# Performance work log

Measured on AMD Instinct MI355X. Metric: run time of the kernel, lower is better.

Reference implementation:

```python
import jax, jax.numpy as jnp
import numpy as np

N, C, INTER = 8192, 256, 128


def setup_inputs() -> dict:
    key = jax.random.key(0)
    ks = jax.random.split(key, 9)
    s_in = 1.0 / np.sqrt(C)
    s_mid = 1.0 / np.sqrt(INTER)
    return {
        "x": jax.random.normal(ks[0], (N, C), dtype=jnp.float32),
        # weights stored [in, out] so projection is x @ w + b
        "g_w": jax.random.uniform(ks[1], (C, INTER), jnp.float32, -s_in, s_in),
        "g_b": jax.random.uniform(ks[2], (INTER,), jnp.float32, -s_in, s_in),
        "theta_w": jax.random.uniform(ks[3], (C, INTER), jnp.float32, -s_in, s_in),
        "theta_b": jax.random.uniform(ks[4], (INTER,), jnp.float32, -s_in, s_in),
        "phi_w": jax.random.uniform(ks[5], (C, INTER), jnp.float32, -s_in, s_in),
        "phi_b": jax.random.uniform(ks[6], (INTER,), jnp.float32, -s_in, s_in),
        "W_w": jax.random.uniform(ks[7], (INTER, C), jnp.float32, -s_mid, s_mid),
        "W_b": jax.random.uniform(ks[8], (C,), jnp.float32, -s_mid, s_mid),
    }


def reference(x, g_w, g_b, theta_w, theta_b, phi_w, phi_b, W_w, W_b):
    # embedded_gaussian variant; dropout treated as eval-mode identity
    g_x = x @ g_w + g_b            # [N, inter]
    theta_x = x @ theta_w + theta_b  # [N, inter]
    phi_x = x @ phi_w + phi_b        # [N, inter]
    f = theta_x @ phi_x.T            # [N, N] score matrix
    f_div_C = jax.nn.softmax(f, axis=-1)
    y = f_div_C @ g_x                # [N, inter]
    W_y = y @ W_w + W_b              # [N, C]
    return W_y + x
```

## Files before the change

kernel.cpp:

```cpp
#include <hip/hip_runtime.h>


typedef __bf16 bf16x8 __attribute__((ext_vector_type(8)));
typedef __bf16 bf16x4 __attribute__((ext_vector_type(4)));
typedef float f32x16 __attribute__((ext_vector_type(16)));

#define DEV __device__ __forceinline__

constexpr int NROW = 8192;
constexpr int CDIM = 256;
constexpr int DI   = 128;
constexpr int KVS  = 8;

DEV int crow(int r, int h) { return (r & 3) + 8 * (r >> 2) + 4 * h; }

DEV f32x16 mfma(bf16x8 a, bf16x8 b, f32x16 c) {
    return __builtin_amdgcn_mfma_f32_32x32x16_bf16(a, b, c, 0, 0, 0);
}

__global__ __launch_bounds__(256, 2) void proj_nt(
    const float* __restrict__ x, const float* __restrict__ w,
    const float* __restrict__ bias, __bf16* __restrict__ out)
{
    __shared__ __align__(16) __bf16 Wl[CDIM * DI];
    const int tid = threadIdx.x;
    const int wv = tid >> 6, lane = tid & 63, l31 = lane & 31, h = lane >> 5;

#pragma unroll
    for (int j = 0; j < 32; ++j) {
        int cid = j * 256 + tid;
        float4 v = ((const float4*)w)[cid];
        bf16x4 t;
        t[0] = (__bf16)v.x; t[1] = (__bf16)v.y; t[2] = (__bf16)v.z; t[3] = (__bf16)v.w;
        *(bf16x4*)(&Wl[cid * 4]) = t;
    }
    __syncthreads();

    const int row0 = blockIdx.x * 128 + wv * 32;
    f32x16 acc[4] = {};

#pragma unroll
    for (int kk = 0; kk < 16; ++kk) {
        const float4* xp = (const float4*)(x + (size_t)(row0 + l31) * CDIM + kk * 16 + h * 8);
        float4 a0 = xp[0], a1 = xp[1];
        bf16x8 af;
        af[0] = (__bf16)a0.x; af[1] = (__bf16)a0.y; af[2] = (__bf16)a0.z; af[3] = (__bf16)a0.w;
        af[4] = (__bf16)a1.x; af[5] = (__bf16)a1.y; af[6] = (__bf16)a1.z; af[7] = (__bf16)a1.w;
#pragma unroll
        for (int jn = 0; jn < 4; ++jn) {
            bf16x8 bf;
#pragma unroll
            for (int u = 0; u < 8; ++u)
                bf[u] = Wl[(kk * 16 + h * 8 + u) * DI + jn * 32 + l31];
            acc[jn] = mfma(af, bf, acc[jn]);
        }
    }

#pragma unroll
    for (int jn = 0; jn < 4; ++jn) {
        int col = jn * 32 + l31;
        float bv = bias[col];
#pragma unroll
        for (int r = 0; r < 16; ++r) {
            int row = row0 + crow(r, h);
            out[(size_t)row * DI + col] = (__bf16)(acc[jn][r] + bv);
        }
    }
}

__global__ __launch_bounds__(256, 2) void proj_gT(
    const float* __restrict__ x, const float* __restrict__ w,
    const float* __restrict__ bias, __bf16* __restrict__ outT)
{
    __shared__ __align__(16) __bf16 Wl[CDIM * DI];
    const int tid = threadIdx.x;
    const int wv = tid >> 6, lane = tid & 63, l31 = lane & 31, h = lane >> 5;

#pragma unroll
    for (int j = 0; j < 32; ++j) {
        int cid = j * 256 + tid;
        float4 v = ((const float4*)w)[cid];
        bf16x4 t;
        t[0] = (__bf16)v.x; t[1] = (__bf16)v.y; t[2] = (__bf16)v.z; t[3] = (__bf16)v.w;
        *(bf16x4*)(&Wl[cid * 4]) = t;
    }
    __syncthreads();

    const int n0 = blockIdx.x * 128;
    f32x16 acc[4] = {};

#pragma unroll
    for (int kk = 0; kk < 16; ++kk) {
        bf16x8 af;
#pragma unroll
        for (int u = 0; u < 8; ++u)
            af[u] = Wl[(kk * 16 + h * 8 + u) * DI + wv * 32 + l31];
#pragma unroll
        for (int jn = 0; jn < 4; ++jn) {
            const float4* xp = (const float4*)(x + (size_t)(n0 + jn * 32 + l31) * CDIM + kk * 16 + h * 8);
            float4 b0 = xp[0], b1 = xp[1];
            bf16x8 bf;
            bf[0] = (__bf16)b0.x; bf[1] = (__bf16)b0.y; bf[2] = (__bf16)b0.z; bf[3] = (__bf16)b0.w;
            bf[4] = (__bf16)b1.x; bf[5] = (__bf16)b1.y; bf[6] = (__bf16)b1.z; bf[7] = (__bf16)b1.w;
            acc[jn] = mfma(af, bf, acc[jn]);
        }
    }

#pragma unroll
    for (int jn = 0; jn < 4; ++jn) {
        int xr = n0 + jn * 32 + l31;
#pragma unroll
        for (int r = 0; r < 16; ++r) {
            int i = wv * 32 + crow(r, h);
            outT[(size_t)i * NROW + xr] = (__bf16)(acc[jn][r] + bias[i]);
        }
    }
}

__global__ __launch_bounds__(256, 2) void flash(
    const __bf16* __restrict__ q, const __bf16* __restrict__ k,
    const __bf16* __restrict__ vT, float* __restrict__ yaccT,
    float* __restrict__ mlm, float* __restrict__ mll)
{
    __shared__ __align__(16) __bf16 Kt[64 * 128];
    __shared__ __align__(16) __bf16 Vt[64 * 128];
    __shared__ __align__(16) __bf16 Pl[4][32 * 64];

    const int tid = threadIdx.x;
    const int wv = tid >> 6, lane = tid & 63, l31 = lane & 31, h = lane >> 5;
    const int qt = blockIdx.x, sp = blockIdx.y;
    const int q0 = qt * 128 + wv * 32;

    bf16x8 qf[8];
#pragma unroll
    for (int kk = 0; kk < 8; ++kk)
        qf[kk] = *(const bf16x8*)(q + (size_t)(q0 + l31) * DI + kk * 16 + h * 8);

    f32x16 yacc[4] = {};
    float m = -1e30f, l = 0.f;

    for (int it = 0; it < 16; ++it) {
        const int kvb = sp * (NROW / KVS) + it * 64;

#pragma unroll
        for (int j = 0; j < 4; ++j) {
            int cid = j * 256 + tid;
            int r = cid >> 4, dc = (cid & 15) * 8;
            bf16x8 val = *(const bf16x8*)(k + (size_t)(kvb + r) * DI + dc);
            *(bf16x8*)(&Kt[(r * 128 + dc) ^ ((r & 15) << 3)]) = val;
        }
#pragma unroll
        for (int j = 0; j < 4; ++j) {
            int cid = j * 256 + tid;
            int d = cid >> 3, kvc = (cid & 7) * 8;
            bf16x8 val = *(const bf16x8*)(vT + (size_t)d * NROW + kvb + kvc);
            int rw = d >> 1, co = (d & 1) * 64 + kvc;
            *(bf16x8*)(&Vt[(rw * 128 + co) ^ ((rw & 15) << 3)]) = val;
        }
        __syncthreads();

        f32x16 sacc[2] = {};
#pragma unroll
        for (int kk = 0; kk < 8; ++kk) {
#pragma unroll
            for (int jm = 0; jm < 2; ++jm) {
                int kv = jm * 32 + l31;
                bf16x8 kf = *(const bf16x8*)(&Kt[(kv * 128 + kk * 16 + h * 8) ^ ((kv & 15) << 3)]);
                sacc[jm] = mfma(kf, qf[kk], sacc[jm]);
            }
        }

        float tm = -1e30f;
#pragma unroll
        for (int jm = 0; jm < 2; ++jm)
#pragma unroll
            for (int r = 0; r < 16; ++r) tm = fmaxf(tm, sacc[jm][r]);
        tm = fmaxf(tm, __shfl_xor(tm, 32));
        float mn = fmaxf(m, tm);
        float scale = __expf(m - mn);
        float ts = 0.f;
#pragma unroll
        for (int jm = 0; jm < 2; ++jm)
#pragma unroll
            for (int r = 0; r < 16; ++r) {
                float p = __expf(sacc[jm][r] - mn);
                sacc[jm][r] = p;
                ts += p;
            }
        ts += __shfl_xor(ts, 32);
        m = mn;
        l = l * scale + ts;
#pragma unroll
        for (int jd = 0; jd < 4; ++jd) yacc[jd] *= scale;

#pragma unroll
        for (int jm = 0; jm < 2; ++jm)
#pragma unroll
            for (int r = 0; r < 16; ++r) {
                int kv = jm * 32 + crow(r, h);
                Pl[wv][(l31 * 64 + kv) ^ ((l31 & 7) << 3)] = (__bf16)sacc[jm][r];
            }
        __syncthreads();

        bf16x8 pf[4];
#pragma unroll
        for (int ks = 0; ks < 4; ++ks)
            pf[ks] = *(const bf16x8*)(&Pl[wv][(l31 * 64 + ks * 16 + h * 8) ^ ((l31 & 7) << 3)]);
#pragma unroll
        for (int jd = 0; jd < 4; ++jd) {
            int d = jd * 32 + l31, rw = d >> 1;
#pragma unroll
            for (int ks = 0; ks < 4; ++ks) {
                int co = (d & 1) * 64 + ks * 16 + h * 8;
                bf16x8 vf = *(const bf16x8*)(&Vt[(rw * 128 + co) ^ ((rw & 15) << 3)]);
                yacc[jd] = mfma(vf, pf[ks], yacc[jd]);
            }
        }
        __syncthreads();
    }

#pragma unroll
    for (int jd = 0; jd < 4; ++jd)
#pragma unroll
        for (int r = 0; r < 16; ++r) {
            int d = jd * 32 + crow(r, h);
            yaccT[(size_t)sp * DI * NROW + (size_t)d * NROW + qt * 128 + wv * 32 + l31] = yacc[jd][r];
        }
    if (h == 0) {
        mlm[sp * NROW + q0 + l31] = m;
        mll[sp * NROW + q0 + l31] = l;
    }
}

__global__ void merge_y(const float* __restrict__ yaccT,
                        const float* __restrict__ mlm, const float* __restrict__ mll,
                        __bf16* __restrict__ y)
{
    int idx = blockIdx.x * 256 + threadIdx.x;
    int d = idx >> 13, qq = idx & 8191;
    float ms[KVS];
    float m = -1e30f;
#pragma unroll
    for (int s = 0; s < KVS; ++s) {
        ms[s] = mlm[s * NROW + qq];
        m = fmaxf(m, ms[s]);
    }
    float L = 0.f, acc = 0.f;
#pragma unroll
    for (int s = 0; s < KVS; ++s) {
        float e = __expf(ms[s] - m);
        L += mll[s * NROW + qq] * e;
        acc += e * yaccT[(size_t)s * DI * NROW + (size_t)d * NROW + qq];
    }
    y[(size_t)qq * DI + d] = (__bf16)(acc / L);
}

__global__ __launch_bounds__(256, 2) void final_proj(
    const __bf16* __restrict__ y, const float* __restrict__ w,
    const float* __restrict__ bias, const float* __restrict__ x,
    float* __restrict__ out)
{
    __shared__ __align__(16) __bf16 Wl[DI * CDIM];
    const int tid = threadIdx.x;
    const int wv = tid >> 6, lane = tid & 63, l31 = lane & 31, h = lane >> 5;

#pragma unroll
    for (int j = 0; j < 32; ++j) {
        int cid = j * 256 + tid;
        float4 v = ((const float4*)w)[cid];
        bf16x4 t;
        t[0] = (__bf16)v.x; t[1] = (__bf16)v.y; t[2] = (__bf16)v.z; t[3] = (__bf16)v.w;
        *(bf16x4*)(&Wl[cid * 4]) = t;
    }
    __syncthreads();

    const int row0 = blockIdx.x * 128 + wv * 32;
    bf16x8 af[8];
#pragma unroll
    for (int kk = 0; kk < 8; ++kk)
        af[kk] = *(const bf16x8*)(y + (size_t)(row0 + l31) * DI + kk * 16 + h * 8);

    f32x16 acc[8] = {};
#pragma unroll
    for (int kk = 0; kk < 8; ++kk) {
#pragma unroll
        for (int jn = 0; jn < 8; ++jn) {
            bf16x8 bf;
#pragma unroll
            for (int u = 0; u < 8; ++u)
                bf[u] = Wl[(kk * 16 + h * 8 + u) * CDIM + jn * 32 + l31];
            acc[jn] = mfma(af[kk], bf, acc[jn]);
        }
    }

#pragma unroll
    for (int jn = 0; jn < 8; ++jn) {
        int col = jn * 32 + l31;
        float bv = bias[col];
#pragma unroll
        for (int r = 0; r < 16; ++r) {
            int row = row0 + crow(r, h);
            out[(size_t)row * CDIM + col] = acc[jn][r] + bv + x[(size_t)row * CDIM + col];
        }
    }
}

extern "C" void kernel_launch(void* const* d_in, const int* in_sizes, int n_in,
                              void* d_out, int out_size, void* d_ws, size_t ws_size,
                              hipStream_t stream)
{
    const float* x    = (const float*)d_in[0];
    const float* g_w  = (const float*)d_in[1];
    const float* g_b  = (const float*)d_in[2];
    const float* th_w = (const float*)d_in[3];
    const float* th_b = (const float*)d_in[4];
    const float* ph_w = (const float*)d_in[5];
    const float* ph_b = (const float*)d_in[6];
    const float* W_w  = (const float*)d_in[7];
    const float* W_b  = (const float*)d_in[8];
    float* out = (float*)d_out;

    char* ws = (char*)d_ws;
    __bf16* qws  = (__bf16*)(ws);
    __bf16* kws  = (__bf16*)(ws + (2ull << 20));
    __bf16* vTws = (__bf16*)(ws + (4ull << 20));
    __bf16* yws  = (__bf16*)(ws + (6ull << 20));
    float*  mlm  = (float*)(ws + (8ull << 20));
    float*  mll  = (float*)(ws + (8ull << 20) + (256ull << 10));
    float*  yac  = (float*)(ws + (9ull << 20));

    proj_nt<<<64, 256, 0, stream>>>(x, th_w, th_b, qws);
    proj_nt<<<64, 256, 0, stream>>>(x, ph_w, ph_b, kws);
    proj_gT<<<64, 256, 0, stream>>>(x, g_w, g_b, vTws);
    flash<<<dim3(64, KVS), 256, 0, stream>>>(qws, kws, vTws, yac, mlm, mll);
    merge_y<<<4096, 256, 0, stream>>>(yac, mlm, mll, yws);
    final_proj<<<64, 256, 0, stream>>>(yws, W_w, W_b, x, out);
}
```

Measured before the change: 188.5 us.

## Fuse projections, prefetch KV in registers, lazy rescale, shuffle P, split KV finer

Merges the three input projections into one launch using a y-grid index. In the flash kernel, the next K/V tile is prefetched into registers during compute, P is kept in registers via cross-half shuffles instead of an LDS round trip, and the running max is only rescaled when it grows by more than a threshold. KV splits rise from 8 to 16 for more parallelism, partial outputs are stored in bf16, and merge_y handles two queries per thread. final_proj uses 256 smaller blocks. Together these trade some partial-sum precision and more merge work for fewer launches, less LDS traffic and better occupancy.

Measured after the change: 307.2 us. 63.0% more time.

```diff
diff --git a/kernel.cpp b/kernel.cpp
--- a/kernel.cpp
+++ b/kernel.cpp
@@ -3,6 +3,7 @@
 
 typedef __bf16 bf16x8 __attribute__((ext_vector_type(8)));
 typedef __bf16 bf16x4 __attribute__((ext_vector_type(4)));
+typedef __bf16 bf16x2 __attribute__((ext_vector_type(2)));
 typedef float f32x16 __attribute__((ext_vector_type(16)));
 
 #define DEV __device__ __forceinline__
@@ -10,7 +11,8 @@
 constexpr int NROW = 8192;
 constexpr int CDIM = 256;
 constexpr int DI   = 128;
-constexpr int KVS  = 8;
+constexpr int KVS  = 16;
+constexpr int NIT  = NROW / KVS / 64;
 
 DEV int crow(int r, int h) { return (r & 3) + 8 * (r >> 2) + 4 * h; }
 
@@ -18,11 +20,24 @@
     return __builtin_amdgcn_mfma_f32_32x32x16_bf16(a, b, c, 0, 0, 0);
 }
 
-__global__ __launch_bounds__(256, 2) void proj_nt(
-    const float* __restrict__ x, const float* __restrict__ w,
-    const float* __restrict__ bias, __bf16* __restrict__ out)
+DEV unsigned pack2(float a, float b) {
+    union { __bf16 h[2]; unsigned u; } t;
+    t.h[0] = (__bf16)a; t.h[1] = (__bf16)b;
+    return t.u;
+}
+
+__global__ __launch_bounds__(256, 2) void proj3(
+    const float* __restrict__ x,
+    const float* __restrict__ thw, const float* __restrict__ thb,
+    const float* __restrict__ phw, const float* __restrict__ phb,
+    const float* __restrict__ gw,  const float* __restrict__ gb,
+    __bf16* __restrict__ qo, __bf16* __restrict__ ko, __bf16* __restrict__ vT)
 {
     __shared__ __align__(16) __bf16 Wl[CDIM * DI];
+    const int which = blockIdx.y;
+    const float* w    = which == 0 ? thw : which == 1 ? phw : gw;
+    const float* bias = which == 0 ? thb : which == 1 ? phb : gb;
+
     const int tid = threadIdx.x;
     const int wv = tid >> 6, lane = tid & 63, l31 = lane & 31, h = lane >> 5;
 
@@ -36,43 +51,257 @@
     }
     __syncthreads();
 
-    const int row0 = blockIdx.x * 128 + wv * 32;
-    f32x16 acc[4] = {};
-
-#pragma unroll
-    for (int kk = 0; kk < 16; ++kk) {
-        const float4* xp = (const float4*)(x + (size_t)(row0 + l31) * CDIM + kk * 16 + h * 8);
-        float4 a0 = xp[0], a1 = xp[1];
-        bf16x8 af;
-        af[0] = (__bf16)a0.x; af[1] = (__bf16)a0.y; af[2] = (__bf16)a0.z; af[3] = (__bf16)a0.w;
-        af[4] = (__bf16)a1.x; af[5] = (__bf16)a1.y; af[6] = (__bf16)a1.z; af[7] = (__bf16)a1.w;
+    if (which < 2) {
+        __bf16* out = which == 0 ? qo : ko;
+        const int row0 = blockIdx.x * 128 + wv * 32;
+        f32x16 acc[4] = {};
+#pragma unroll
+        for (int kk = 0; kk < 16; ++kk) {
+            const float4* xp = (const float4*)(x + (size_t)(row0 + l31) * CDIM + kk * 16 + h * 8);
+            float4 a0 = xp[0], a1 = xp[1];
+            bf16x8 af;
+            af[0] = (__bf16)a0.x; af[1] = (__bf16)a0.y; af[2] = (__bf16)a0.z; af[3] = (__bf16)a0.w;
+            af[4] = (__bf16)a1.x; af[5] = (__bf16)a1.y; af[6] = (__bf16)a1.z; af[7] = (__bf16)a1.w;
+#pragma unroll
+            for (int jn = 0; jn < 4; ++jn) {
+                bf16x8 bf;
+#pragma unroll
+                for (int u = 0; u < 8; ++u)
+                    bf[u] = Wl[(kk * 16 + h * 8 + u) * DI + jn * 32 + l31];
+                acc[jn] = mfma(af, bf, acc[jn]);
+            }
+        }
 #pragma unroll
         for (int jn = 0; jn < 4; ++jn) {
-            bf16x8 bf;
+            int col = jn * 32 + l31;
+            float bv = bias[col];
+#pragma unroll
+            for (int r = 0; r < 16; ++r)
+                out[(size_t)(row0 + crow(r, h)) * DI + col] = (__bf16)(acc[jn][r] + bv);
+        }
+    } else {
+        const int n0 = blockIdx.x * 128;
+        f32x16 acc[4] = {};
+#pragma unroll
+        for (int kk = 0; kk < 16; ++kk) {
+            bf16x8 af;
 #pragma unroll
             for (int u = 0; u < 8; ++u)
-                bf[u] = Wl[(kk * 16 + h * 8 + u) * DI + jn * 32 + l31];
-            acc[jn] = mfma(af, bf, acc[jn]);
-        }
-    }
-
-#pragma unroll
-    for (int jn = 0; jn < 4; ++jn) {
-        int col = jn * 32 + l31;
-        float bv = bias[col];
+                af[u] = Wl[(kk * 16 + h * 8 + u) * DI + wv * 32 + l31];
+#pragma unroll
+            for (int jn = 0; jn < 4; ++jn) {
+                const float4* xp = (const float4*)(x + (size_t)(n0 + jn * 32 + l31) * CDIM + kk * 16 + h * 8);
+                float4 b0 = xp[0], b1 = xp[1];
+                bf16x8 bf;
+                bf[0] = (__bf16)b0.x; bf[1] = (__bf16)b0.y; bf[2] = (__bf16)b0.z; bf[3] = (__bf16)b0.w;
+                bf[4] = (__bf16)b1.x; bf[5] = (__bf16)b1.y; bf[6] = (__bf16)b1.z; bf[7] = (__bf16)b1.w;
+                acc[jn] = mfma(af, bf, acc[jn]);
+            }
+        }
+#pragma unroll
+        for (int jn = 0; jn < 4; ++jn) {
+            int xr = n0 + jn * 32 + l31;
+#pragma unroll
+            for (int r = 0; r < 16; ++r) {
+                int i = wv * 32 + crow(r, h);
+                vT[(size_t)i * NROW + xr] = (__bf16)(acc[jn][r] + bias[i]);
+            }
+        }
+    }
+}
+
+__global__ __launch_bounds__(256, 3) void flash(
+    const __bf16* __restrict__ q, const __bf16* __restrict__ k,
+    const __bf16* __restrict__ vT, __bf16* __restrict__ yaccT,
+    float* __restrict__ mlm, float* __restrict__ mll)
+{
+    __shared__ __align__(16) __bf16 Kt[64 * 128];
+    __shared__ __align__(16) __bf16 Vt[64 * 128];
+
+    const int tid = threadIdx.x;
+    const int wv = tid >> 6, lane = tid & 63, l31 = lane & 31, h = lane >> 5;
+    const int qt = blockIdx.x, sp = blockIdx.y;
+    const int q0 = qt * 128 + wv * 32;
+
+    bf16x8 qf[8];
+#pragma unroll
+    for (int kk = 0; kk < 8; ++kk)
+        qf[kk] = *(const bf16x8*)(q + (size_t)(q0 + l31) * DI + kk * 16 + h * 8);
+
+    f32x16 yacc[4] = {};
+    float m = -1e30f, l = 0.f;
+
+    bf16x8 kr[4], vr[4];
+    {
+        const int kvb = sp * (NROW / KVS);
+#pragma unroll
+        for (int j = 0; j < 4; ++j) {
+            int cid = j * 256 + tid, r = cid >> 4, dc = (cid & 15) * 8;
+            kr[j] = *(const bf16x8*)(k + (size_t)(kvb + r) * DI + dc);
+        }
+#pragma unroll
+        for (int j = 0; j < 4; ++j) {
+            int cid = j * 256 + tid, d = cid >> 3, kvc = (cid & 7) * 8;
+            vr[j] = *(const bf16x8*)(vT + (size_t)d * NROW + kvb + kvc);
+        }
+#pragma unroll
+        for (int j = 0; j < 4; ++j) {
+            int cid = j * 256 + tid, r = cid >> 4, dc = (cid & 15) * 8;
+            *(bf16x8*)(&Kt[(r * 128 + dc) ^ ((r & 15) << 3)]) = kr[j];
+        }
+#pragma unroll
+        for (int j = 0; j < 4; ++j) {
+            int cid = j * 256 + tid, d = cid >> 3, kvc = (cid & 7) * 8;
+            int rw = d >> 1, co = (d & 1) * 64 + kvc;
+            *(bf16x8*)(&Vt[(rw * 128 + co) ^ ((rw & 15) << 3)]) = vr[j];
+        }
+    }
+    __syncthreads();
+
+    for (int it = 0; it < NIT; ++it) {
+        const int kvb_n = sp * (NROW / KVS) + (it < NIT - 1 ? (it + 1) * 64 : it * 64);
+#pragma unroll
+        for (int j = 0; j < 4; ++j) {
+            int cid = j * 256 + tid, r = cid >> 4, dc = (cid & 15) * 8;
+            kr[j] = *(const bf16x8*)(k + (size_t)(kvb_n + r) * DI + dc);
+        }
+#pragma unroll
+        for (int j = 0; j < 4; ++j) {
+            int cid = j * 256 + tid, d = cid >> 3, kvc = (cid & 7) * 8;
+            vr[j] = *(const bf16x8*)(vT + (size_t)d * NROW + kvb_n + kvc);
+        }
+
+        f32x16 sacc[2] = {};
+#pragma unroll
+        for (int kk = 0; kk < 8; ++kk) {
+#pragma unroll
+            for (int jm = 0; jm < 2; ++jm) {
+                int kv = jm * 32 + l31;
+                bf16x8 kf = *(const bf16x8*)(&Kt[(kv * 128 + kk * 16 + h * 8) ^ ((kv & 15) << 3)]);
+                sacc[jm] = mfma(kf, qf[kk], sacc[jm]);
+            }
+        }
+
+        float tm = -1e30f;
+#pragma unroll
+        for (int jm = 0; jm < 2; ++jm)
+#pragma unroll
+            for (int r = 0; r < 16; ++r) tm = fmaxf(tm, sacc[jm][r]);
+        tm = fmaxf(tm, __shfl_xor(tm, 32));
+        if (!__all(tm <= m + 8.f)) {
+            float mn = fmaxf(m, tm);
+            float sc = __expf(m - mn);
+            l *= sc;
+#pragma unroll
+            for (int jd = 0; jd < 4; ++jd) yacc[jd] *= sc;
+            m = mn;
+        }
+        float ts = 0.f;
+#pragma unroll
+        for (int jm = 0; jm < 2; ++jm)
+#pragma unroll
+            for (int r = 0; r < 16; ++r) {
+                float p = __expf(sacc[jm][r] - m);
+                sacc[jm][r] = p;
+                ts += p;
+            }
+        ts += __shfl_xor(ts, 32);
+        l += ts;
+
+        bf16x8 pf[4];
+#pragma unroll
+        for (int ks = 0; ks < 4; ++ks) {
+            const int jm = ks >> 1, r0 = 8 * (ks & 1);
+            unsigned a0 = pack2(sacc[jm][r0],     sacc[jm][r0 + 1]);
+            unsigned a1 = pack2(sacc[jm][r0 + 2], sacc[jm][r0 + 3]);
+            unsigned b0 = pack2(sacc[jm][r0 + 4], sacc[jm][r0 + 5]);
+            unsigned b1 = pack2(sacc[jm][r0 + 6], sacc[jm][r0 + 7]);
+            unsigned snd0 = h ? a0 : b0, snd1 = h ? a1 : b1;
+            unsigned loc0 = h ? b0 : a0, loc1 = h ? b1 : a1;
+            unsigned rcv0 = (unsigned)__shfl_xor((int)snd0, 32);
+            unsigned rcv1 = (unsigned)__shfl_xor((int)snd1, 32);
+            union { unsigned w[4]; bf16x8 v; } pu;
+            pu.w[0] = h ? rcv0 : loc0;
+            pu.w[1] = h ? rcv1 : loc1;
+            pu.w[2] = h ? loc0 : rcv0;
+            pu.w[3] = h ? loc1 : rcv1;
+            pf[ks] = pu.v;
+        }
+
+#pragma unroll
+        for (int jd = 0; jd < 4; ++jd) {
+            int d = jd * 32 + l31, rw = d >> 1;
+#pragma unroll
+            for (int ks = 0; ks < 4; ++ks) {
+                int co = (d & 1) * 64 + ks * 16 + h * 8;
+                bf16x8 vf = *(const bf16x8*)(&Vt[(rw * 128 + co) ^ ((rw & 15) << 3)]);
+                yacc[jd] = mfma(vf, pf[ks], yacc[jd]);
+            }
+        }
+        __syncthreads();
+
+        if (it < NIT - 1) {
+#pragma unroll
+            for (int j = 0; j < 4; ++j) {
+                int cid = j * 256 + tid, r = cid >> 4, dc = (cid & 15) * 8;
+                *(bf16x8*)(&Kt[(r * 128 + dc) ^ ((r & 15) << 3)]) = kr[j];
+            }
+#pragma unroll
+            for (int j = 0; j < 4; ++j) {
+                int cid = j * 256 + tid, d = cid >> 3, kvc = (cid & 7) * 8;
+                int rw = d >> 1, co = (d & 1) * 64 + kvc;
+                *(bf16x8*)(&Vt[(rw * 128 + co) ^ ((rw & 15) << 3)]) = vr[j];
+            }
+        }
+        __syncthreads();
+    }
+
+#pragma unroll
+    for (int jd = 0; jd < 4; ++jd)
 #pragma unroll
         for (int r = 0; r < 16; ++r) {
-            int row = row0 + crow(r, h);
-            out[(size_t)row * DI + col] = (__bf16)(acc[jn][r] + bv);
-        }
-    }
-}
-
-__global__ __launch_bounds__(256, 2) void proj_gT(
-    const float* __restrict__ x, const float* __restrict__ w,
-    const float* __restrict__ bias, __bf16* __restrict__ outT)
-{
-    __shared__ __align__(16) __bf16 Wl[CDIM * DI];
+            int d = jd * 32 + crow(r, h);
+            yaccT[(size_t)sp * DI * NROW + (size_t)d * NROW + qt * 128 + wv * 32 + l31] =
+                (__bf16)yacc[jd][r];
+        }
+    if (h == 0) {
+        mlm[sp * NROW + q0 + l31] = m;
+        mll[sp * NROW + q0 + l31] = l;
+    }
+}
+
+__global__ void merge_y(const __bf16* __restrict__ yaccT,
+                        const float* __restrict__ mlm, const float* __restrict__ mll,
+                        __bf16* __restrict__ y)
+{
+    int idx = blockIdx.x * 256 + threadIdx.x;
+    int d = idx >> 12, q2 = (idx & 4095) * 2;
+    float2 mv[KVS];
+    float m0 = -1e30f, m1 = -1e30f;
+#pragma unroll
+    for (int s = 0; s < KVS; ++s) {
+        mv[s] = *(const float2*)(mlm + s * NROW + q2);
+        m0 = fmaxf(m0, mv[s].x); m1 = fmaxf(m1, mv[s].y);
+    }
+    float L0 = 0.f, L1 = 0.f, a0 = 0.f, a1 = 0.f;
+#pragma unroll
+    for (int s = 0; s < KVS; ++s) {
+        float2 lv = *(const float2*)(mll + s * NROW + q2);
+        float e0 = __expf(mv[s].x - m0), e1 = __expf(mv[s].y - m1);
+        L0 += lv.x * e0; L1 += lv.y * e1;
+        bf16x2 pv = *(const bf16x2*)(yaccT + (size_t)s * DI * NROW + (size_t)d * NROW + q2);
+        a0 += e0 * (float)pv[0]; a1 += e1 * (float)pv[1];
+    }
+    y[(size_t)q2 * DI + d]       = (__bf16)(a0 / L0);
+    y[(size_t)(q2 + 1) * DI + d] = (__bf16)(a1 / L1);
+}
+
+__global__ __launch_bounds__(256, 2) void final_proj(
+    const __bf16* __restrict__ y, const float* __restrict__ w,
+    const float* __restrict__ bias, const float* __restrict__ x,
+    float* __restrict__ out)
+{
+    __shared__ __align__(16) __bf16 Wl[DI * CDIM];
     const int tid = threadIdx.x;
     const int wv = tid >> 6, lane = tid & 63, l31 = lane & 31, h = lane >> 5;
 
@@ -86,216 +315,29 @@
     }
     __syncthreads();
 
-    const int n0 = blockIdx.x * 128;
-    f32x16 acc[4] = {};
-
-#pragma unroll
-    for (int kk = 0; kk < 16; ++kk) {
-        bf16x8 af;
-#pragma unroll
-        for (int u = 0; u < 8; ++u)
-            af[u] = Wl[(kk * 16 + h * 8 + u) * DI + wv * 32 + l31];
-#pragma unroll
-        for (int jn = 0; jn < 4; ++jn) {
-            const float4* xp = (const float4*)(x + (size_t)(n0 + jn * 32 + l31) * CDIM + kk * 16 + h * 8);
-            float4 b0 = xp[0], b1 = xp[1];
-            bf16x8 bf;
-            bf[0] = (__bf16)b0.x; bf[1] = (__bf16)b0.y; bf[2] = (__bf16)b0.z; bf[3] = (__bf16)b0.w;
-            bf[4] = (__bf16)b1.x; bf[5] = (__bf16)b1.y; bf[6] = (__bf16)b1.z; bf[7] = (__bf16)b1.w;
-            acc[jn] = mfma(af, bf, acc[jn]);
-        }
-    }
-
-#pragma unroll
-    for (int jn = 0; jn < 4; ++jn) {
-        int xr = n0 + jn * 32 + l31;
-#pragma unroll
-        for (int r = 0; r < 16; ++r) {
-            int i = wv * 32 + crow(r, h);
-            outT[(size_t)i * NROW + xr] = (__bf16)(acc[jn][r] + bias[i]);
-        }
-    }
-}
-
-__global__ __launch_bounds__(256, 2) void flash(
-    const __bf16* __restrict__ q, const __bf16* __restrict__ k,
-    const __bf16* __restrict__ vT, float* __restrict__ yaccT,
-    float* __restrict__ mlm, float* __restrict__ mll)
-{
-    __shared__ __align__(16) __bf16 Kt[64 * 128];
-    __shared__ __align__(16) __bf16 Vt[64 * 128];
-    __shared__ __align__(16) __bf16 Pl[4][32 * 64];
-
-    const int tid = threadIdx.x;
-    const int wv = tid >> 6, lane = tid & 63, l31 = lane & 31, h = lane >> 5;
-    const int qt = blockIdx.x, sp = blockIdx.y;
-    const int q0 = qt * 128 + wv * 32;
-
-    bf16x8 qf[8];
-#pragma unroll
-    for (int kk = 0; kk < 8; ++kk)
-        qf[kk] = *(const bf16x8*)(q + (size_t)(q0 + l31) * DI + kk * 16 + h * 8);
-
-    f32x16 yacc[4] = {};
-    float m = -1e30f, l = 0.f;
-
-    for (int it = 0; it < 16; ++it) {
-        const int kvb = sp * (NROW / KVS) + it * 64;
-
-#pragma unroll
-        for (int j = 0; j < 4; ++j) {
-            int cid = j * 256 + tid;
-            int r = cid >> 4, dc = (cid & 15) * 8;
-            bf16x8 val = *(const bf16x8*)(k + (size_t)(kvb + r) * DI + dc);
-            *(bf16x8*)(&Kt[(r * 128 + dc) ^ ((r & 15) << 3)]) = val;
-        }
-#pragma unroll
-        for (int j = 0; j < 4; ++j) {
-            int cid = j * 256 + tid;
-            int d = cid >> 3, kvc = (cid & 7) * 8;
-            bf16x8 val = *(const bf16x8*)(vT + (size_t)d * NROW + kvb + kvc);
-            int rw = d >> 1, co = (d & 1) * 64 + kvc;
-            *(bf16x8*)(&Vt[(rw * 128 + co) ^ ((rw & 15) << 3)]) = val;
-        }
-        __syncthreads();
-
-        f32x16 sacc[2] = {};
-#pragma unroll
-        for (int kk = 0; kk < 8; ++kk) {
-#pragma unroll
-            for (int jm = 0; jm < 2; ++jm) {
-                int kv = jm * 32 + l31;
-                bf16x8 kf = *(const bf16x8*)(&Kt[(kv * 128 + kk * 16 + h * 8) ^ ((kv & 15) << 3)]);
-                sacc[jm] = mfma(kf, qf[kk], sacc[jm]);
-            }
-        }
-
-        float tm = -1e30f;
-#pragma unroll
-        for (int jm = 0; jm < 2; ++jm)
-#pragma unroll
-            for (int r = 0; r < 16; ++r) tm = fmaxf(tm, sacc[jm][r]);
-        tm = fmaxf(tm, __shfl_xor(tm, 32));
-        float mn = fmaxf(m, tm);
-        float scale = __expf(m - mn);
-        float ts = 0.f;
-#pragma unroll
-        for (int jm = 0; jm < 2; ++jm)
-#pragma unroll
-            for (int r = 0; r < 16; ++r) {
-                float p = __expf(sacc[jm][r] - mn);
-                sacc[jm][r] = p;
-                ts += p;
-            }
-        ts += __shfl_xor(ts, 32);
-        m = mn;
-        l = l * scale + ts;
-#pragma unroll
-        for (int jd = 0; jd < 4; ++jd) yacc[jd] *= scale;
-
-#pragma unroll
-        for (int jm = 0; jm < 2; ++jm)
-#pragma unroll
-            for (int r = 0; r < 16; ++r) {
-                int kv = jm * 32 + crow(r, h);
-                Pl[wv][(l31 * 64 + kv) ^ ((l31 & 7) << 3)] = (__bf16)sacc[jm][r];
-            }
-        __syncthreads();
-
-        bf16x8 pf[4];
-#pragma unroll
-        for (int ks = 0; ks < 4; ++ks)
-            pf[ks] = *(const bf16x8*)(&Pl[wv][(l31 * 64 + ks * 16 + h * 8) ^ ((l31 & 7) << 3)]);
-#pragma unroll
-        for (int jd = 0; jd < 4; ++jd) {
-            int d = jd * 32 + l31, rw = d >> 1;
-#pragma unroll
-            for (int ks = 0; ks < 4; ++ks) {
-                int co = (d & 1) * 64 + ks * 16 + h * 8;
-                bf16x8 vf = *(const bf16x8*)(&Vt[(rw * 128 + co) ^ ((rw & 15) << 3)]);
-                yacc[jd] = mfma(vf, pf[ks], yacc[jd]);
-            }
-        }
-        __syncthreads();
-    }
-
-#pragma unroll
-    for (int jd = 0; jd < 4; ++jd)
-#pragma unroll
-        for (int r = 0; r < 16; ++r) {
-            int d = jd * 32 + crow(r, h);
-            yaccT[(size_t)sp * DI * NROW + (size_t)d * NROW + qt * 128 + wv * 32 + l31] = yacc[jd][r];
-        }
-    if (h == 0) {
-        mlm[sp * NROW + q0 + l31] = m;
-        mll[sp * NROW + q0 + l31] = l;
-    }
-}
-
-__global__ void merge_y(const float* __restrict__ yaccT,
-                        const float* __restrict__ mlm, const float* __restrict__ mll,
-                        __bf16* __restrict__ y)
-{
-    int idx = blockIdx.x * 256 + threadIdx.x;
-    int d = idx >> 13, qq = idx & 8191;
-    float ms[KVS];
-    float m = -1e30f;
-#pragma unroll
-    for (int s = 0; s < KVS; ++s) {
-        ms[s] = mlm[s * NROW + qq];
-        m = fmaxf(m, ms[s]);
-    }
-    float L = 0.f, acc = 0.f;
-#pragma unroll
-    for (int s = 0; s < KVS; ++s) {
-        float e = __expf(ms[s] - m);
-        L += mll[s * NROW + qq] * e;
-        acc += e * yaccT[(size_t)s * DI * NROW + (size_t)d * NROW + qq];
-    }
-    y[(size_t)qq * DI + d] = (__bf16)(acc / L);
-}
-
-__global__ __launch_bounds__(256, 2) void final_proj(
-    const __bf16* __restrict__ y, const float* __restrict__ w,
-    const float* __restrict__ bias, const float* __restrict__ x,
-    float* __restrict__ out)
-{
-    __shared__ __align__(16) __bf16 Wl[DI * CDIM];
-    const int tid = threadIdx.x;
-    const int wv = tid >> 6, lane = tid & 63, l31 = lane & 31, h = lane >> 5;
-
-#pragma unroll
-    for (int j = 0; j < 32; ++j) {
-        int cid = j * 256 + tid;
-        float4 v = ((const float4*)w)[cid];
-        bf16x4 t;
-        t[0] = (__bf16)v.x; t[1] = (__bf16)v.y; t[2] = (__bf16)v.z; t[3] = (__bf16)v.w;
-        *(bf16x4*)(&Wl[cid * 4]) = t;
-    }
-    __syncthreads();
-
-    const int row0 = blockIdx.x * 128 + wv * 32;
+    const int row0 = blockIdx.x * 32;
     bf16x8 af[8];
 #pragma unroll
     for (int kk = 0; kk < 8; ++kk)
         af[kk] = *(const bf16x8*)(y + (size_t)(row0 + l31) * DI + kk * 16 + h * 8);
 
-    f32x16 acc[8] = {};
+    f32x16 acc[2] = {};
 #pragma unroll
     for (int kk = 0; kk < 8; ++kk) {
 #pragma unroll
-        for (int jn = 0; jn < 8; ++jn) {
+        for (int jn = 0; jn < 2; ++jn) {
+            int col0 = (wv * 2 + jn) * 32;
             bf16x8 bf;
 #pragma unroll
             for (int u = 0; u < 8; ++u)
-                bf[u] = Wl[(kk * 16 + h * 8 + u) * CDIM + jn * 32 + l31];
+                bf[u] = Wl[(kk * 16 + h * 8 + u) * CDIM + col0 + l31];
             acc[jn] = mfma(af[kk], bf, acc[jn]);
         }
     }
 
 #pragma unroll
-    for (int jn = 0; jn < 8; ++jn) {
-        int col = jn * 32 + l31;
+    for (int jn = 0; jn < 2; ++jn) {
+        int col = (wv * 2 + jn) * 32 + l31;
         float bv = bias[col];
 #pragma unroll
         for (int r = 0; r < 16; ++r) {
@@ -326,13 +368,12 @@
     __bf16* vTws = (__bf16*)(ws + (4ull << 20));
     __bf16* yws  = (__bf16*)(ws + (6ull << 20));
     float*  mlm  = (float*)(ws + (8ull << 20));
-    float*  mll  = (float*)(ws + (8ull << 20) + (256ull << 10));
-    float*  yac  = (float*)(ws + (9ull << 20));
-
-    proj_nt<<<64, 256, 0, stream>>>(x, th_w, th_b, qws);
-    proj_nt<<<64, 256, 0, stream>>>(x, ph_w, ph_b, kws);
-    proj_gT<<<64, 256, 0, stream>>>(x, g_w, g_b, vTws);
+    float*  mll  = (float*)(ws + (8ull << 20) + (512ull << 10));
+    __bf16* yac  = (__bf16*)(ws + (9ull << 20));
+
+    proj3<<<dim3(64, 3), 256, 0, stream>>>(x, th_w, th_b, ph_w, ph_b, g_w, g_b,
+                                           qws, kws, vTws);
     flash<<<dim3(64, KVS), 256, 0, stream>>>(qws, kws, vTws, yac, mlm, mll);
-    merge_y<<<4096, 256, 0, stream>>>(yac, mlm, mll, yws);
-    final_proj<<<64, 256, 0, stream>>>(yws, W_w, W_b, x, out);
-}
+    merge_y<<<2048, 256, 0, stream>>>(yac, mlm, mll, yws);
+    final_proj<<<256, 256, 0, stream>>>(yws, W_w, W_b, x, out);
+}
```
